# Kernel optimization log

Measured on AMD Instinct MI355X. Metric: run time of the kernel, lower is better.

Reference implementation:

```python
import jax, jax.numpy as jnp
import numpy as np

B, T, C = 512, 256, 192
HEAD = 64

def setup_inputs() -> dict:
    key = jax.random.key(0)
    ks = jax.random.split(key, 5)
    return {
        "x": jax.random.normal(ks[0], (B, T, C), dtype=jnp.float32),
        "Wk": jax.random.normal(ks[1], (C, HEAD), dtype=jnp.float32) * (C ** -0.5),
        "Wq": jax.random.normal(ks[2], (C, HEAD), dtype=jnp.float32) * (C ** -0.5),
        "Wv": jax.random.normal(ks[3], (C, HEAD), dtype=jnp.float32) * (C ** -0.5),
        "pos_table": jax.random.normal(ks[4], (T, C), dtype=jnp.float32),
    }

def reference(x, Wk, Wq, Wv, pos_table):
    Bx, Tx, Cx = x.shape
    scale = Cx ** -0.5  # note: scales by n_embed, not head_size (faithful to source)
    k = jnp.einsum('btc,ch->bth', x, Wk)
    q = jnp.einsum('btc,ch->bth', x, Wq)
    v = jnp.einsum('btc,ch->bth', x, Wv)
    pe = pos_table[:Tx]                       # [T, C]
    pos_k = pe @ Wk                           # [T, H]
    pos_q = pe @ Wq                           # [T, H]
    bias = pos_k @ pos_q.T                    # [T, T]
    wei = jnp.einsum('bqh,bkh->bqk', q, k) * scale + bias
    causal = jnp.tril(jnp.ones((Tx, Tx), dtype=bool))
    wei = jnp.where(causal, wei, -jnp.inf)
    wei = jax.nn.softmax(wei, axis=-1)
    # dropout is identity in inference mode
    out = jnp.einsum('bqk,bkh->bqh', wei, v)
    return out
```

## Files before the change

kernel.cpp:

```cpp
#include <hip/hip_runtime.h>
#include <hip/hip_bf16.h>

typedef unsigned short u16;
typedef unsigned int u32;
using bf16x8 = __attribute__((ext_vector_type(8))) short;
using f32x4  = __attribute__((ext_vector_type(4))) float;

#define BB 512
#define TT 256
#define CC 192
#define HH 64

__device__ __forceinline__ u16 f2bf(float f) {
    __hip_bfloat16 h = __float2bfloat16(f);
    u16 u; __builtin_memcpy(&u, &h, 2); return u;
}


__global__ void wprep_kernel(const float* __restrict__ Wq,
                             const float* __restrict__ Wk,
                             const float* __restrict__ Wv,
                             u16* __restrict__ W_sw) {
    int gid  = blockIdx.x * 256 + threadIdx.x;
    int fid  = gid >> 6, lane = gid & 63;
    int n3   = fid / 6,  ks   = fid % 6;
    int l15  = lane & 15, quad = lane >> 4;
    const float* W = (n3 < 4) ? Wq : (n3 < 8) ? Wk : Wv;
    const int h = (n3 & 3) * 16 + l15;
    u16* dst = W_sw + (size_t)gid * 8;
    #pragma unroll
    for (int u = 0; u < 8; ++u) {
        int c = ks * 32 + quad * 8 + u;
        dst[u] = f2bf(W[c * HH + h]);
    }
}

__global__ void pos_kernel(const float* __restrict__ Wk,
                           const float* __restrict__ Wq,
                           const float* __restrict__ pe,
                           float* __restrict__ poskT, float* __restrict__ posqT) {
    int t = blockIdx.x * 4 + (threadIdx.x >> 6);
    int h = threadIdx.x & 63;
    float ak = 0.f, aq = 0.f;
    for (int c = 0; c < CC; ++c) {
        float p = pe[t * CC + c];
        ak += p * Wk[c * HH + h];
        aq += p * Wq[c * HH + h];
    }
    poskT[h * TT + t] = ak;
    posqT[h * TT + t] = aq;
}

__global__ void bias_kernel(const float* __restrict__ poskT,
                            const float* __restrict__ posqT,
                            float4* __restrict__ bias_sw) {
    const int i = blockIdx.x >> 4, jt = blockIdx.x & 15;
    if (jt > i) return;
    const int lane = threadIdx.x;
    const int l15 = lane & 15, quad = lane >> 4;
    const int tq = i * 16 + quad * 4;
    const int jc = jt * 16 + l15;
    float s[4] = {0.f, 0.f, 0.f, 0.f};
    for (int h = 0; h < HH; ++h) {
        float pq = posqT[h * TT + jc];
        #pragma unroll
        for (int r = 0; r < 4; ++r)
            s[r] += poskT[h * TT + tq + r] * pq;
    }
    bias_sw[blockIdx.x * 64 + lane] = make_float4(s[0], s[1], s[2], s[3]);
}


#define XP 200
#define VP 264
#define PP 40
#define P_ELEMS 640
#define WQK_OFF 12800
#define Q_OFF   61952
#define K_OFF   94720
#define V_OFF   127488
#define LDS_TOTAL 161280

__global__ __launch_bounds__(512, 1)
void fused_kernel(const float* __restrict__ x,
                  const u16* __restrict__ W_sw,
                  const float4* __restrict__ bias_sw,
                  float* __restrict__ out) {
    extern __shared__ __align__(16) char smem[];
    u16* Qlds = (u16*)(smem + Q_OFF);
    u16* Klds = (u16*)(smem + K_OFF);
    u16* Vt   = (u16*)(smem + V_OFF);

    const int tid  = threadIdx.x;
    const int w    = tid >> 6;
    const int w4   = w & 3;
    const int mh   = w >> 2;
    const int lane = tid & 63;
    const int l15  = lane & 15;
    const int quad = lane >> 4;
    const int b    = blockIdx.x;

    {
        const uint4* src = (const uint4*)W_sw;
        uint4* dst = (uint4*)(smem + WQK_OFF);
        #pragma unroll
        for (int it = 0; it < 6; ++it)
            dst[it * 512 + tid] = src[it * 512 + tid];
    }

    const bf16x8* Wv8 = (const bf16x8*)W_sw;
    bf16x8 WfV[6];
    #pragma unroll
    for (int ks = 0; ks < 6; ++ks)
        WfV[ks] = Wv8[(((8 + w4) * 6) + ks) * 64 + lane];
    #pragma unroll
    for (int j = 0; j < 6; ++j)
        asm volatile("" : "+v"(WfV[j]));

    const int hs    = w4 >> 1;
    const int quadp = (w4 * 2 + (l15 >> 3)) & 3;
    const int uu    = l15 & 7;

    {
        const float* xb = x + (size_t)b * TT * CC;
        float4 vv[3];
        #pragma unroll
        for (int it = 0; it < 3; ++it)
            vv[it] = *(const float4*)(xb + (it * 512 + tid) * 4);
        u16* xs = (u16*)smem;
        #pragma unroll
        for (int it = 0; it < 3; ++it) {
            const int flat = (it * 512 + tid) * 4;
            const int row = flat / CC, col = flat % CC;
            uint2 pk;
            pk.x = (u32)f2bf(vv[it].x) | ((u32)f2bf(vv[it].y) << 16);
            pk.y = (u32)f2bf(vv[it].z) | ((u32)f2bf(vv[it].w) << 16);
            *(uint2*)&xs[row * XP + col] = pk;
        }
    }
    __syncthreads();

    #pragma unroll 1
    for (int c8 = 0; c8 < 8; ++c8) {
        const bool hn = (c8 < 7);
        float4 vnext[3];
        if (hn) {
            const float* xb = x + ((size_t)b * TT + (c8 + 1) * 32) * CC;
            #pragma unroll
            for (int it = 0; it < 3; ++it)
                vnext[it] = *(const float4*)(xb + (it * 512 + tid) * 4);
        }
        const u16* xs = (const u16*)smem;
        f32x4 acc[3];
        #pragma unroll
        for (int i = 0; i < 3; ++i) acc[i] = {0.f, 0.f, 0.f, 0.f};
        #pragma unroll
        for (int ks = 0; ks < 6; ++ks) {
            const bf16x8 a  = *(const bf16x8*)&xs[(mh * 16 + l15) * XP + ks * 32 + quad * 8];
            const bf16x8 wq = *(const bf16x8*)(smem + WQK_OFF + ((w4 * 6 + ks) * 64 + lane) * 16);
            const bf16x8 wk = *(const bf16x8*)(smem + WQK_OFF + (((4 + w4) * 6 + ks) * 64 + lane) * 16);
            acc[0] = __builtin_amdgcn_mfma_f32_16x16x32_bf16(a, wq, acc[0], 0, 0, 0);
            acc[1] = __builtin_amdgcn_mfma_f32_16x16x32_bf16(a, wk, acc[1], 0, 0, 0);
            acc[2] = __builtin_amdgcn_mfma_f32_16x16x32_bf16(a, WfV[ks], acc[2], 0, 0, 0);
        }
        {
            const int i_loc = c8 * 2 + mh;
            const int base  = (i_loc * 2 + hs) * 512 + (quadp * 16 + quad * 4) * 8 + uu;
            #pragma unroll
            for (int r = 0; r < 4; ++r) {
                Qlds[base + r * 8] = f2bf(acc[0][r]);
                Klds[base + r * 8] = f2bf(acc[1][r]);
            }
            #pragma unroll
            for (int r = 0; r < 4; ++r)
                Vt[(w4 * 16 + l15) * VP + i_loc * 16 + quad * 4 + r]
                    = f2bf(acc[2][r]);
        }
        __syncthreads();
        if (hn) {
            u16* xsn = (u16*)smem;
            #pragma unroll
            for (int it = 0; it < 3; ++it) {
                const int flat = (it * 512 + tid) * 4;
                const int row = flat / CC, col = flat % CC;
                uint2 pk;
                pk.x = (u32)f2bf(vnext[it].x) | ((u32)f2bf(vnext[it].y) << 16);
                pk.y = (u32)f2bf(vnext[it].z) | ((u32)f2bf(vnext[it].w) << 16);
                *(uint2*)&xsn[row * XP + col] = pk;
            }
            __syncthreads();
        }
    }

    u16* Pw = (u16*)smem + w * P_ELEMS;
    const float scale = 0.07216878364870322f;
    const f32x4 zero4 = {0.f, 0.f, 0.f, 0.f};
    const bf16x8* qv = (const bf16x8*)Qlds;
    const bf16x8* kv = (const bf16x8*)Klds;

    #pragma unroll 1
    for (int mt = 0; mt < 2; ++mt) {
        const int i  = mt ? 15 - w : w;
        const int t0 = 16 * i;
        const int J  = i + 1;
        const int Pq = (J + 1) >> 1;

        const bf16x8 qf0 = qv[(i * 2 + 0) * 64 + lane];
        const bf16x8 qf1 = qv[(i * 2 + 1) * 64 + lane];

        f32x4 o[4];
        float m4[4], l4[4];
        #pragma unroll
        for (int n = 0; n < 4; ++n) o[n] = zero4;
        #pragma unroll
        for (int r = 0; r < 4; ++r) { m4[r] = -1e30f; l4[r] = 0.f; }

        #pragma unroll
        for (int p = 0; p < 8; ++p) {
            if (p < Pq) {
                const int jt0 = 2 * p, jt1 = 2 * p + 1;
                f32x4 sa = zero4, sb;
                {
                    bf16x8 k0 = kv[(jt0 * 2 + 0) * 64 + lane];
                    bf16x8 k1 = kv[(jt0 * 2 + 1) * 64 + lane];
                    sa = __builtin_amdgcn_mfma_f32_16x16x32_bf16(qf0, k0, sa, 0, 0, 0);
                    sa = __builtin_amdgcn_mfma_f32_16x16x32_bf16(qf1, k1, sa, 0, 0, 0);
                    const float4 b4 = bias_sw[(i * 16 + jt0) * 64 + lane];
                    sa[0] = sa[0] * scale + b4.x;
                    sa[1] = sa[1] * scale + b4.y;
                    sa[2] = sa[2] * scale + b4.z;
                    sa[3] = sa[3] * scale + b4.w;
                    if (jt0 == i) {
                        #pragma unroll
                        for (int r = 0; r < 4; ++r)
                            if (l15 > quad * 4 + r) sa[r] = -1e30f;
                    }
                }
                if (jt1 < J) {
                    sb = zero4;
                    bf16x8 k0 = kv[(jt1 * 2 + 0) * 64 + lane];
                    bf16x8 k1 = kv[(jt1 * 2 + 1) * 64 + lane];
                    sb = __builtin_amdgcn_mfma_f32_16x16x32_bf16(qf0, k0, sb, 0, 0, 0);
                    sb = __builtin_amdgcn_mfma_f32_16x16x32_bf16(qf1, k1, sb, 0, 0, 0);
                    const float4 b4 = bias_sw[(i * 16 + jt1) * 64 + lane];
                    sb[0] = sb[0] * scale + b4.x;
                    sb[1] = sb[1] * scale + b4.y;
                    sb[2] = sb[2] * scale + b4.z;
                    sb[3] = sb[3] * scale + b4.w;
                    if (jt1 == i) {
                        #pragma unroll
                        for (int r = 0; r < 4; ++r)
                            if (l15 > quad * 4 + r) sb[r] = -1e30f;
                    }
                } else {
                    sb[0] = -1e30f; sb[1] = -1e30f; sb[2] = -1e30f; sb[3] = -1e30f;
                }
                float t4[4];
                #pragma unroll
                for (int r = 0; r < 4; ++r) t4[r] = fmaxf(sa[r], sb[r]);
                #pragma unroll
                for (int d = 1; d < 16; d <<= 1) {
                    #pragma unroll
                    for (int r = 0; r < 4; ++r) t4[r] = fmaxf(t4[r], __shfl_xor(t4[r], d, 64));
                }
                float al[4];
                #pragma unroll
                for (int r = 0; r < 4; ++r) {
                    float mn = fmaxf(m4[r], t4[r]);
                    al[r] = __expf(m4[r] - mn);
                    m4[r] = mn;
                    l4[r] *= al[r];
                }
                #pragma unroll
                for (int n = 0; n < 4; ++n)
                #pragma unroll
                for (int r = 0; r < 4; ++r) o[n][r] *= al[r];
                #pragma unroll
                for (int r = 0; r < 4; ++r) {
                    float e0 = __expf(sa[r] - m4[r]);
                    float e1 = __expf(sb[r] - m4[r]);
                    l4[r] += e0 + e1;
                    Pw[(quad * 4 + r) * PP + l15]      = f2bf(e0);
                    Pw[(quad * 4 + r) * PP + 16 + l15] = f2bf(e1);
                }
                bf16x8 pa = *(const bf16x8*)&Pw[l15 * PP + quad * 8];
                #pragma unroll
                for (int n = 0; n < 4; ++n) {
                    bf16x8 bv = *(const bf16x8*)&Vt[(n * 16 + l15) * VP + p * 32 + quad * 8];
                    o[n] = __builtin_amdgcn_mfma_f32_16x16x32_bf16(pa, bv, o[n], 0, 0, 0);
                }
            }
        }
        #pragma unroll
        for (int d = 1; d < 16; d <<= 1) {
            #pragma unroll
            for (int r = 0; r < 4; ++r) l4[r] += __shfl_xor(l4[r], d, 64);
        }
        float rl4[4];
        #pragma unroll
        for (int r = 0; r < 4; ++r) rl4[r] = 1.f / l4[r];
        float* ob = out + ((size_t)b * TT + t0) * HH;
        #pragma unroll
        for (int n = 0; n < 4; ++n)
        #pragma unroll
        for (int r = 0; r < 4; ++r)
            ob[(quad * 4 + r) * HH + n * 16 + l15] = o[n][r] * rl4[r];
    }
}

extern "C" void kernel_launch(void* const* d_in, const int* in_sizes, int n_in,
                              void* d_out, int out_size, void* d_ws, size_t ws_size,
                              hipStream_t stream) {
    const float* x  = (const float*)d_in[0];
    const float* Wk = (const float*)d_in[1];
    const float* Wq = (const float*)d_in[2];
    const float* Wv = (const float*)d_in[3];
    const float* pe = (const float*)d_in[4];
    float* out = (float*)d_out;

    float*  poskT  = (float*)d_ws;
    float*  posqT  = poskT + TT * HH;
    float4* biassw = (float4*)(posqT + TT * HH);
    u16*    W_sw   = (u16*)((float*)biassw + TT * TT);

    static bool attr_set = false;
    if (!attr_set) {
        hipFuncSetAttribute(reinterpret_cast<const void*>(fused_kernel),
                            hipFuncAttributeMaxDynamicSharedMemorySize, LDS_TOTAL);
        attr_set = true;
    }

    wprep_kernel<<<18, 256, 0, stream>>>(Wq, Wk, Wv, W_sw);
    pos_kernel<<<TT / 4, 256, 0, stream>>>(Wk, Wq, pe, poskT, posqT);
    bias_kernel<<<256, 64, 0, stream>>>(poskT, posqT, biassw);
    fused_kernel<<<BB, 512, LDS_TOTAL, stream>>>(x, W_sw, biassw, out);
}
```

Before: 201.0 us.

## Swizzle LDS layouts, use DPP reductions, merge prep kernels, hoist bias loads

XOR-swizzles the x tile and transposed V tile in LDS to cut bank conflicts, and packs the V stores into 64-bit writes. Replaces the first two shuffle stages of the row max and sum reductions with DPP quad permutes. Merges the weight-prep and positional kernels into one launch to save launch overhead. Also turns the fully unrolled attention loop into a runtime loop with both bias loads issued up front, which shrinks code size but removes unrolling across iterations.

```diff
diff --git a/kernel.cpp b/kernel.cpp
--- a/kernel.cpp
+++ b/kernel.cpp
@@ -16,39 +16,48 @@
     u16 u; __builtin_memcpy(&u, &h, 2); return u;
 }
 
-
-__global__ void wprep_kernel(const float* __restrict__ Wq,
-                             const float* __restrict__ Wk,
-                             const float* __restrict__ Wv,
-                             u16* __restrict__ W_sw) {
-    int gid  = blockIdx.x * 256 + threadIdx.x;
-    int fid  = gid >> 6, lane = gid & 63;
-    int n3   = fid / 6,  ks   = fid % 6;
-    int l15  = lane & 15, quad = lane >> 4;
-    const float* W = (n3 < 4) ? Wq : (n3 < 8) ? Wk : Wv;
-    const int h = (n3 & 3) * 16 + l15;
-    u16* dst = W_sw + (size_t)gid * 8;
-    #pragma unroll
-    for (int u = 0; u < 8; ++u) {
-        int c = ks * 32 + quad * 8 + u;
-        dst[u] = f2bf(W[c * HH + h]);
-    }
-}
-
-__global__ void pos_kernel(const float* __restrict__ Wk,
-                           const float* __restrict__ Wq,
-                           const float* __restrict__ pe,
-                           float* __restrict__ poskT, float* __restrict__ posqT) {
-    int t = blockIdx.x * 4 + (threadIdx.x >> 6);
-    int h = threadIdx.x & 63;
-    float ak = 0.f, aq = 0.f;
-    for (int c = 0; c < CC; ++c) {
-        float p = pe[t * CC + c];
-        ak += p * Wk[c * HH + h];
-        aq += p * Wq[c * HH + h];
-    }
-    poskT[h * TT + t] = ak;
-    posqT[h * TT + t] = aq;
+__device__ __forceinline__ float dpp_x1(float x) {
+    int y = __builtin_amdgcn_update_dpp(0, __float_as_int(x), 0xB1, 0xF, 0xF, true);
+    return __int_as_float(y);
+}
+__device__ __forceinline__ float dpp_x2(float x) {
+    int y = __builtin_amdgcn_update_dpp(0, __float_as_int(x), 0x4E, 0xF, 0xF, true);
+    return __int_as_float(y);
+}
+
+
+__global__ void prep_a(const float* __restrict__ Wq,
+                       const float* __restrict__ Wk,
+                       const float* __restrict__ Wv,
+                       const float* __restrict__ pe,
+                       u16* __restrict__ W_sw,
+                       float* __restrict__ poskT, float* __restrict__ posqT) {
+    if (blockIdx.x < 18) {
+        int gid  = blockIdx.x * 256 + threadIdx.x;
+        int fid  = gid >> 6, lane = gid & 63;
+        int n3   = fid / 6,  ks   = fid % 6;
+        int l15  = lane & 15, quad = lane >> 4;
+        const float* W = (n3 < 4) ? Wq : (n3 < 8) ? Wk : Wv;
+        const int h = (n3 & 3) * 16 + l15;
+        u16* dst = W_sw + (size_t)gid * 8;
+        #pragma unroll
+        for (int u = 0; u < 8; ++u) {
+            int c = ks * 32 + quad * 8 + u;
+            dst[u] = f2bf(W[c * HH + h]);
+        }
+    } else {
+        int bid = blockIdx.x - 18;
+        int t = bid * 4 + (threadIdx.x >> 6);
+        int h = threadIdx.x & 63;
+        float ak = 0.f, aq = 0.f;
+        for (int c = 0; c < CC; ++c) {
+            float p = pe[t * CC + c];
+            ak += p * Wk[c * HH + h];
+            aq += p * Wq[c * HH + h];
+        }
+        poskT[h * TT + t] = ak;
+        posqT[h * TT + t] = aq;
+    }
 }
 
 __global__ void bias_kernel(const float* __restrict__ poskT,
@@ -89,7 +98,7 @@
     extern __shared__ __align__(16) char smem[];
     u16* Qlds = (u16*)(smem + Q_OFF);
     u16* Klds = (u16*)(smem + K_OFF);
-    u16* Vt   = (u16*)(smem + V_OFF);
+    char* VtB = smem + V_OFF;
 
     const int tid  = threadIdx.x;
     const int w    = tid >> 6;
@@ -99,6 +108,7 @@
     const int l15  = lane & 15;
     const int quad = lane >> 4;
     const int b    = blockIdx.x;
+    const int swz  = (l15 & 7) << 4;
 
     {
         const uint4* src = (const uint4*)W_sw;
@@ -127,7 +137,6 @@
         #pragma unroll
         for (int it = 0; it < 3; ++it)
             vv[it] = *(const float4*)(xb + (it * 512 + tid) * 4);
-        u16* xs = (u16*)smem;
         #pragma unroll
         for (int it = 0; it < 3; ++it) {
             const int flat = (it * 512 + tid) * 4;
@@ -135,7 +144,7 @@
             uint2 pk;
             pk.x = (u32)f2bf(vv[it].x) | ((u32)f2bf(vv[it].y) << 16);
             pk.y = (u32)f2bf(vv[it].z) | ((u32)f2bf(vv[it].w) << 16);
-            *(uint2*)&xs[row * XP + col] = pk;
+            *(uint2*)(smem + row * (XP * 2) + ((col * 2) ^ ((row & 7) << 4))) = pk;
         }
     }
     __syncthreads();
@@ -150,13 +159,13 @@
             for (int it = 0; it < 3; ++it)
                 vnext[it] = *(const float4*)(xb + (it * 512 + tid) * 4);
         }
-        const u16* xs = (const u16*)smem;
         f32x4 acc[3];
         #pragma unroll
         for (int i = 0; i < 3; ++i) acc[i] = {0.f, 0.f, 0.f, 0.f};
         #pragma unroll
         for (int ks = 0; ks < 6; ++ks) {
-            const bf16x8 a  = *(const bf16x8*)&xs[(mh * 16 + l15) * XP + ks * 32 + quad * 8];
+            const bf16x8 a  = *(const bf16x8*)(smem + (mh * 16 + l15) * (XP * 2)
+                                               + ((ks * 64 + quad * 16) ^ swz));
             const bf16x8 wq = *(const bf16x8*)(smem + WQK_OFF + ((w4 * 6 + ks) * 64 + lane) * 16);
             const bf16x8 wk = *(const bf16x8*)(smem + WQK_OFF + (((4 + w4) * 6 + ks) * 64 + lane) * 16);
             acc[0] = __builtin_amdgcn_mfma_f32_16x16x32_bf16(a, wq, acc[0], 0, 0, 0);
@@ -171,14 +180,14 @@
                 Qlds[base + r * 8] = f2bf(acc[0][r]);
                 Klds[base + r * 8] = f2bf(acc[1][r]);
             }
-            #pragma unroll
-            for (int r = 0; r < 4; ++r)
-                Vt[(w4 * 16 + l15) * VP + i_loc * 16 + quad * 4 + r]
-                    = f2bf(acc[2][r]);
+            uint2 pv;
+            pv.x = (u32)f2bf(acc[2][0]) | ((u32)f2bf(acc[2][1]) << 16);
+            pv.y = (u32)f2bf(acc[2][2]) | ((u32)f2bf(acc[2][3]) << 16);
+            *(uint2*)(VtB + (w4 * 16 + l15) * (VP * 2)
+                      + ((i_loc * 32 + quad * 8) ^ swz)) = pv;
         }
         __syncthreads();
         if (hn) {
-            u16* xsn = (u16*)smem;
             #pragma unroll
             for (int it = 0; it < 3; ++it) {
                 const int flat = (it * 512 + tid) * 4;
@@ -186,7 +195,7 @@
                 uint2 pk;
                 pk.x = (u32)f2bf(vnext[it].x) | ((u32)f2bf(vnext[it].y) << 16);
                 pk.y = (u32)f2bf(vnext[it].z) | ((u32)f2bf(vnext[it].w) << 16);
-                *(uint2*)&xsn[row * XP + col] = pk;
+                *(uint2*)(smem + row * (XP * 2) + ((col * 2) ^ ((row & 7) << 4))) = pk;
             }
             __syncthreads();
         }
@@ -215,86 +224,89 @@
         #pragma unroll
         for (int r = 0; r < 4; ++r) { m4[r] = -1e30f; l4[r] = 0.f; }
 
-        #pragma unroll
-        for (int p = 0; p < 8; ++p) {
-            if (p < Pq) {
-                const int jt0 = 2 * p, jt1 = 2 * p + 1;
-                f32x4 sa = zero4, sb;
-                {
-                    bf16x8 k0 = kv[(jt0 * 2 + 0) * 64 + lane];
-                    bf16x8 k1 = kv[(jt0 * 2 + 1) * 64 + lane];
-                    sa = __builtin_amdgcn_mfma_f32_16x16x32_bf16(qf0, k0, sa, 0, 0, 0);
-                    sa = __builtin_amdgcn_mfma_f32_16x16x32_bf16(qf1, k1, sa, 0, 0, 0);
-                    const float4 b4 = bias_sw[(i * 16 + jt0) * 64 + lane];
-                    sa[0] = sa[0] * scale + b4.x;
-                    sa[1] = sa[1] * scale + b4.y;
-                    sa[2] = sa[2] * scale + b4.z;
-                    sa[3] = sa[3] * scale + b4.w;
-                    if (jt0 == i) {
-                        #pragma unroll
-                        for (int r = 0; r < 4; ++r)
-                            if (l15 > quad * 4 + r) sa[r] = -1e30f;
-                    }
+        #pragma unroll 1
+        for (int p = 0; p < Pq; ++p) {
+            const int jt0 = 2 * p, jt1 = 2 * p + 1;
+            const float4 b4a = bias_sw[(i * 16 + jt0) * 64 + lane];
+            const float4 b4b = bias_sw[(i * 16 + jt1) * 64 + lane];
+            f32x4 sa = zero4, sb;
+            {
+                bf16x8 k0 = kv[(jt0 * 2 + 0) * 64 + lane];
+                bf16x8 k1 = kv[(jt0 * 2 + 1) * 64 + lane];
+                sa = __builtin_amdgcn_mfma_f32_16x16x32_bf16(qf0, k0, sa, 0, 0, 0);
+                sa = __builtin_amdgcn_mfma_f32_16x16x32_bf16(qf1, k1, sa, 0, 0, 0);
+                sa[0] = sa[0] * scale + b4a.x;
+                sa[1] = sa[1] * scale + b4a.y;
+                sa[2] = sa[2] * scale + b4a.z;
+                sa[3] = sa[3] * scale + b4a.w;
+                if (jt0 == i) {
+                    #pragma unroll
+                    for (int r = 0; r < 4; ++r)
+                        if (l15 > quad * 4 + r) sa[r] = -1e30f;
                 }
-                if (jt1 < J) {
-                    sb = zero4;
-                    bf16x8 k0 = kv[(jt1 * 2 + 0) * 64 + lane];
-                    bf16x8 k1 = kv[(jt1 * 2 + 1) * 64 + lane];
-                    sb = __builtin_amdgcn_mfma_f32_16x16x32_bf16(qf0, k0, sb, 0, 0, 0);
-                    sb = __builtin_amdgcn_mfma_f32_16x16x32_bf16(qf1, k1, sb, 0, 0, 0);
-                    const float4 b4 = bias_sw[(i * 16 + jt1) * 64 + lane];
-                    sb[0] = sb[0] * scale + b4.x;
-                    sb[1] = sb[1] * scale + b4.y;
-                    sb[2] = sb[2] * scale + b4.z;
-                    sb[3] = sb[3] * scale + b4.w;
-                    if (jt1 == i) {
-                        #pragma unroll
-                        for (int r = 0; r < 4; ++r)
-                            if (l15 > quad * 4 + r) sb[r] = -1e30f;
-                    }
-                } else {
-                    sb[0] = -1e30f; sb[1] = -1e30f; sb[2] = -1e30f; sb[3] = -1e30f;
+            }
+            if (jt1 < J) {
+                sb = zero4;
+                bf16x8 k0 = kv[(jt1 * 2 + 0) * 64 + lane];
+                bf16x8 k1 = kv[(jt1 * 2 + 1) * 64 + lane];
+                sb = __builtin_amdgcn_mfma_f32_16x16x32_bf16(qf0, k0, sb, 0, 0, 0);
+                sb = __builtin_amdgcn_mfma_f32_16x16x32_bf16(qf1, k1, sb, 0, 0, 0);
+                sb[0] = sb[0] * scale + b4b.x;
+                sb[1] = sb[1] * scale + b4b.y;
+                sb[2] = sb[2] * scale + b4b.z;
+                sb[3] = sb[3] * scale + b4b.w;
+                if (jt1 == i) {
+                    #pragma unroll
+                    for (int r = 0; r < 4; ++r)
+                        if (l15 > quad * 4 + r) sb[r] = -1e30f;
                 }
-                float t4[4];
-                #pragma unroll
-                for (int r = 0; r < 4; ++r) t4[r] = fmaxf(sa[r], sb[r]);
-                #pragma unroll
-                for (int d = 1; d < 16; d <<= 1) {
-                    #pragma unroll
-                    for (int r = 0; r < 4; ++r) t4[r] = fmaxf(t4[r], __shfl_xor(t4[r], d, 64));
-                }
-                float al[4];
-                #pragma unroll
-                for (int r = 0; r < 4; ++r) {
-                    float mn = fmaxf(m4[r], t4[r]);
-                    al[r] = __expf(m4[r] - mn);
-                    m4[r] = mn;
-                    l4[r] *= al[r];
-                }
-                #pragma unroll
-                for (int n = 0; n < 4; ++n)
-                #pragma unroll
-                for (int r = 0; r < 4; ++r) o[n][r] *= al[r];
-                #pragma unroll
-                for (int r = 0; r < 4; ++r) {
-                    float e0 = __expf(sa[r] - m4[r]);
-                    float e1 = __expf(sb[r] - m4[r]);
-                    l4[r] += e0 + e1;
-                    Pw[(quad * 4 + r) * PP + l15]      = f2bf(e0);
-                    Pw[(quad * 4 + r) * PP + 16 + l15] = f2bf(e1);
-                }
-                bf16x8 pa = *(const bf16x8*)&Pw[l15 * PP + quad * 8];
-                #pragma unroll
-                for (int n = 0; n < 4; ++n) {
-                    bf16x8 bv = *(const bf16x8*)&Vt[(n * 16 + l15) * VP + p * 32 + quad * 8];
-                    o[n] = __builtin_amdgcn_mfma_f32_16x16x32_bf16(pa, bv, o[n], 0, 0, 0);
-                }
-            }
-        }
-        #pragma unroll
-        for (int d = 1; d < 16; d <<= 1) {
-            #pragma unroll
-            for (int r = 0; r < 4; ++r) l4[r] += __shfl_xor(l4[r], d, 64);
+            } else {
+                sb[0] = -1e30f; sb[1] = -1e30f; sb[2] = -1e30f; sb[3] = -1e30f;
+            }
+            float t4[4];
+            #pragma unroll
+            for (int r = 0; r < 4; ++r) t4[r] = fmaxf(sa[r], sb[r]);
+            #pragma unroll
+            for (int r = 0; r < 4; ++r) {
+                t4[r] = fmaxf(t4[r], dpp_x1(t4[r]));
+                t4[r] = fmaxf(t4[r], dpp_x2(t4[r]));
+                t4[r] = fmaxf(t4[r], __shfl_xor(t4[r], 4, 64));
+                t4[r] = fmaxf(t4[r], __shfl_xor(t4[r], 8, 64));
+            }
+            float al[4];
+            #pragma unroll
+            for (int r = 0; r < 4; ++r) {
+                float mn = fmaxf(m4[r], t4[r]);
+                al[r] = __expf(m4[r] - mn);
+                m4[r] = mn;
+                l4[r] *= al[r];
+            }
+            #pragma unroll
+            for (int n = 0; n < 4; ++n)
+            #pragma unroll
+            for (int r = 0; r < 4; ++r) o[n][r] *= al[r];
+            #pragma unroll
+            for (int r = 0; r < 4; ++r) {
+                float e0 = __expf(sa[r] - m4[r]);
+                float e1 = __expf(sb[r] - m4[r]);
+                l4[r] += e0 + e1;
+                Pw[(quad * 4 + r) * PP + l15]      = f2bf(e0);
+                Pw[(quad * 4 + r) * PP + 16 + l15] = f2bf(e1);
+            }
+            bf16x8 pa = *(const bf16x8*)&Pw[l15 * PP + quad * 8];
+            #pragma unroll
+            for (int n = 0; n < 4; ++n) {
+                bf16x8 bv = *(const bf16x8*)(VtB + (n * 16 + l15) * (VP * 2)
+                                             + ((p * 64 + quad * 16) ^ swz));
+                o[n] = __builtin_amdgcn_mfma_f32_16x16x32_bf16(pa, bv, o[n], 0, 0, 0);
+            }
+        }
+        #pragma unroll
+        for (int r = 0; r < 4; ++r) {
+            l4[r] += dpp_x1(l4[r]);
+            l4[r] += dpp_x2(l4[r]);
+            l4[r] += __shfl_xor(l4[r], 4, 64);
+            l4[r] += __shfl_xor(l4[r], 8, 64);
         }
         float rl4[4];
         #pragma unroll
@@ -330,8 +342,7 @@
         attr_set = true;
     }
 
-    wprep_kernel<<<18, 256, 0, stream>>>(Wq, Wk, Wv, W_sw);
-    pos_kernel<<<TT / 4, 256, 0, stream>>>(Wk, Wq, pe, poskT, posqT);
+    prep_a<<<18 + TT / 4, 256, 0, stream>>>(Wq, Wk, Wv, pe, W_sw, poskT, posqT);
     bias_kernel<<<256, 64, 0, stream>>>(poskT, posqT, biassw);
     fused_kernel<<<BB, 512, LDS_TOTAL, stream>>>(x, W_sw, biassw, out);
 }
```

Result: no change. 197.6 us (-1.7%).
